# Optimization experiments

Measured on AMD Instinct MI355X. Metric: run time of the kernel, lower is better.

## Reference

```python
import jax, jax.numpy as jnp
import numpy as np

B, S, DIM, HEADS, MLP = 2, 2048, 1024, 16, 4096
DH = DIM // HEADS
LN_EPS = 1e-5


def layernorm(x, g, b):
    m = x.mean(-1, keepdims=True)
    v = ((x - m) ** 2).mean(-1, keepdims=True)
    return (x - m) / jnp.sqrt(v + LN_EPS) * g + b


def rope(x):
    # x: [B, H, S, dh]; interleaved-pair RoPE (rotary_embedding_torch convention)
    dh = x.shape[-1]
    s = x.shape[-2]
    inv_freq = 1.0 / (10000.0 ** (jnp.arange(0, dh, 2, dtype=jnp.float32) / dh))
    freqs = jnp.arange(s, dtype=jnp.float32)[:, None] * inv_freq[None, :]  # [S, dh/2]
    cos = jnp.repeat(jnp.cos(freqs), 2, axis=-1)  # [S, dh]
    sin = jnp.repeat(jnp.sin(freqs), 2, axis=-1)
    xp = x.reshape(x.shape[:-1] + (dh // 2, 2))
    x_rot = jnp.stack([-xp[..., 1], xp[..., 0]], axis=-1).reshape(x.shape)
    return x * cos + x_rot * sin


def setup_inputs() -> dict:
    key = jax.random.key(0)
    ks = jax.random.split(key, 10)
    w = 0.02
    return {
        "x": jax.random.normal(ks[0], (B, S, DIM), jnp.float32),
        "bias": jax.random.normal(ks[1], (B, S, S), jnp.float32) * 0.1,
        "ln1_g": jnp.ones((DIM,), jnp.float32),
        "ln1_b": jnp.zeros((DIM,), jnp.float32),
        "W_qkv": jax.random.normal(ks[2], (DIM, 3 * DIM), jnp.float32) * w,
        "W_o": jax.random.normal(ks[3], (DIM, DIM), jnp.float32) * w,
        "ln2_g": jnp.ones((DIM,), jnp.float32),
        "ln2_b": jnp.zeros((DIM,), jnp.float32),
        "W1": jax.random.normal(ks[4], (DIM, MLP), jnp.float32) * w,
        "b1": jnp.zeros((MLP,), jnp.float32),
        "W2": jax.random.normal(ks[5], (MLP, DIM), jnp.float32) * w,
        "b2": jnp.zeros((DIM,), jnp.float32),
        "pad_mask": jnp.zeros((B, S), jnp.int32),
    }


def reference(x, bias, ln1_g, ln1_b, W_qkv, W_o, ln2_g, ln2_b, W1, b1, W2, b2, pad_mask):
    b, s, d = x.shape
    h, dh = HEADS, DH
    res = x
    x1 = layernorm(x, ln1_g, ln1_b)
    qkv = (x1 @ W_qkv).reshape(b, s, h, 3 * dh)
    q, k, v = jnp.split(qkv, 3, axis=-1)            # each [B,S,H,dh]
    q = rope(q.transpose(0, 2, 1, 3))               # [B,H,S,dh]
    k = rope(k.transpose(0, 2, 1, 3))
    v = v.transpose(0, 2, 1, 3)
    scores = jnp.einsum("bhqd,bhkd->bhqk", q, k) * (dh ** -0.5)
    scores = scores + bias[:, None]                 # additive bias per batch
    key_mask = pad_mask.astype(bool)[:, None, None, :]
    scores = jnp.where(key_mask, -jnp.inf, scores)
    attn = jax.nn.softmax(scores, axis=-1)          # dropout = identity (eval)
    out = jnp.einsum("bhqk,bhkd->bhqd", attn, v)
    out = out.transpose(0, 2, 1, 3).reshape(b, s, d)
    x = res + out @ W_o
    res2 = x
    x2 = layernorm(x, ln2_g, ln2_b)
    mlp = jax.nn.gelu(x2 @ W1 + b1, approximate=False) @ W2 + b2
    return res2 + mlp
```

## Files before the change

kernel.cpp:

```cpp
#include <hip/hip_runtime.h>
#include <hip/hip_bf16.h>

#define B_   2
#define S_   2048
#define DIM_ 1024
#define H_   16
#define DH_  64
#define MLP_ 4096

typedef __bf16 bf16x8 __attribute__((ext_vector_type(8)));
typedef float  f32x4  __attribute__((ext_vector_type(4)));

__device__ __forceinline__ ushort f2bf(float f) {
    union { float f; unsigned u; } x; x.f = f;
    unsigned r = x.u + 0x7FFFu + ((x.u >> 16) & 1u);
    return (ushort)(r >> 16);
}
__device__ __forceinline__ float bf2f(ushort b) {
    union { unsigned u; float f; } x; x.u = ((unsigned)b) << 16;
    return x.f;
}

#define GLOAD_LDS16(gptr, lptr)                                                        \
    __builtin_amdgcn_global_load_lds(                                                  \
        (const __attribute__((address_space(1))) unsigned int*)(const void*)(gptr),    \
        (__attribute__((address_space(3))) unsigned int*)(void*)(lptr), 16, 0, 0)

#define MFMA_BF16(a, b, c) __builtin_amdgcn_mfma_f32_16x16x32_bf16((a), (b), (c), 0, 0, 0)

__global__ __launch_bounds__(256) void transpose_cvt(const float* __restrict__ in,
                                                     ushort* __restrict__ out,
                                                     int K, int N) {
    __shared__ float t[32][33];
    int n0 = blockIdx.x * 32, k0 = blockIdx.y * 32;
    int tx = threadIdx.x, ty = threadIdx.y;
#pragma unroll
    for (int r = 0; r < 32; r += 8)
        t[ty + r][tx] = in[(size_t)(k0 + ty + r) * N + n0 + tx];
    __syncthreads();
#pragma unroll
    for (int r = 0; r < 32; r += 8)
        out[(size_t)(n0 + ty + r) * K + k0 + tx] = f2bf(t[tx][ty + r]);
}

__global__ __launch_bounds__(256) void vt_prep(const ushort* __restrict__ qkv,
                                               ushort* __restrict__ VT) {
    __shared__ ushort t[32][34];
    int s0 = blockIdx.x * 32, d0 = blockIdx.y * 32, bh = blockIdx.z;
    int h = bh & 15, b = bh >> 4;
    const ushort* src = qkv + (size_t)b * S_ * (3 * DIM_) + h * 192 + 128;
    int tx = threadIdx.x, ty = threadIdx.y;
#pragma unroll
    for (int r = 0; r < 32; r += 8)
        t[ty + r][tx] = src[(size_t)(s0 + ty + r) * (3 * DIM_) + d0 + tx];
    __syncthreads();
    ushort* dst = VT + ((size_t)bh * DH_ + d0) * S_ + s0;
#pragma unroll
    for (int r = 0; r < 32; r += 8)
        dst[(size_t)(ty + r) * S_ + tx] = t[tx][ty + r];
}

__global__ __launch_bounds__(256) void ln_kernel(const float* __restrict__ in,
                                                 const float* __restrict__ g,
                                                 const float* __restrict__ beta,
                                                 ushort* __restrict__ out) {
    int row = blockIdx.x;
    float4 v = reinterpret_cast<const float4*>(in + (size_t)row * DIM_)[threadIdx.x];
    float s = v.x + v.y + v.z + v.w;
    float s2 = v.x * v.x + v.y * v.y + v.z * v.z + v.w * v.w;
#pragma unroll
    for (int m = 1; m < 64; m <<= 1) { s += __shfl_xor(s, m); s2 += __shfl_xor(s2, m); }
    __shared__ float red[8];
    int wid = threadIdx.x >> 6;
    if ((threadIdx.x & 63) == 0) { red[wid] = s; red[4 + wid] = s2; }
    __syncthreads();
    s  = red[0] + red[1] + red[2] + red[3];
    s2 = red[4] + red[5] + red[6] + red[7];
    float mean = s * (1.f / DIM_);
    float var  = s2 * (1.f / DIM_) - mean * mean;
    float inv  = rsqrtf(var + 1e-5f);
    float4 gg = reinterpret_cast<const float4*>(g)[threadIdx.x];
    float4 bb = reinterpret_cast<const float4*>(beta)[threadIdx.x];
    ushort4 o;
    o.x = f2bf((v.x - mean) * inv * gg.x + bb.x);
    o.y = f2bf((v.y - mean) * inv * gg.y + bb.y);
    o.z = f2bf((v.z - mean) * inv * gg.z + bb.z);
    o.w = f2bf((v.w - mean) * inv * gg.w + bb.w);
    reinterpret_cast<ushort4*>(out + (size_t)row * DIM_)[threadIdx.x] = o;
}

template <bool BIAS, bool GELU, bool RES, bool OBF16>
__global__ __launch_bounds__(256) void gemm_bt(const ushort* __restrict__ A,
                                               const ushort* __restrict__ Bt,
                                               void* __restrict__ Cout,
                                               const float* __restrict__ bias,
                                               const float* __restrict__ resid,
                                               int M, int N, int K) {
    __shared__ __align__(16) ushort As[2][128 * 32];
    __shared__ __align__(16) ushort Bs[2][128 * 32];
    int tid = threadIdx.x;
    int wid = tid >> 6, lane = tid & 63;
    int lr = lane & 15, lg = lane >> 4;

    int nbx = gridDim.x;
    int nwg = nbx * gridDim.y;
    int bid = blockIdx.y * nbx + blockIdx.x;
    int swz = (bid & 7) * (nwg >> 3) + (bid >> 3);
    int row0 = (swz / nbx) * 128, col0 = (swz % nbx) * 128;

    int wm = (wid >> 1) * 64, wn = (wid & 1) * 64;
    int srow = tid >> 2, scol = (tid & 3) * 8;

    f32x4 acc[4][4] = {};

    const ushort* ga0 = A + (size_t)(row0 + srow) * K + scol;
    const ushort* ga1 = A + (size_t)(row0 + 64 + srow) * K + scol;
    const ushort* gb0 = Bt + (size_t)(col0 + srow) * K + scol;
    const ushort* gb1 = Bt + (size_t)(col0 + 64 + srow) * K + scol;

    auto stage = [&](int buf, int kt) {
        ushort* a = As[buf] + wid * 512;
        ushort* b = Bs[buf] + wid * 512;
        GLOAD_LDS16(ga0 + kt, a);
        GLOAD_LDS16(ga1 + kt, a + 2048);
        GLOAD_LDS16(gb0 + kt, b);
        GLOAD_LDS16(gb1 + kt, b + 2048);
    };

    int nk = K >> 5;
    stage(0, 0);
    __syncthreads();

    for (int t = 0; t < nk; t++) {
        int cur = t & 1;
        if (t + 1 < nk) stage(cur ^ 1, (t + 1) << 5);
        bf16x8 af[4], bfr[4];
#pragma unroll
        for (int m = 0; m < 4; m++)
            af[m] = *reinterpret_cast<const bf16x8*>(As[cur] + (wm + m * 16 + lr) * 32 + lg * 8);
#pragma unroll
        for (int n = 0; n < 4; n++)
            bfr[n] = *reinterpret_cast<const bf16x8*>(Bs[cur] + (wn + n * 16 + lr) * 32 + lg * 8);
#pragma unroll
        for (int m = 0; m < 4; m++)
#pragma unroll
            for (int n = 0; n < 4; n++)
                acc[m][n] = MFMA_BF16(af[m], bfr[n], acc[m][n]);
        __syncthreads();
    }

#pragma unroll
    for (int m = 0; m < 4; m++) {
#pragma unroll
        for (int n = 0; n < 4; n++) {
            int col = col0 + wn + n * 16 + lr;
#pragma unroll
            for (int i = 0; i < 4; i++) {
                int row = row0 + wm + m * 16 + lg * 4 + i;
                float v = acc[m][n][i];
                if (BIAS) v += bias[col];
                if (GELU) v = 0.5f * v * (1.f + erff(v * 0.70710678118f));
                if (RES)  v += resid[(size_t)row * N + col];
                if (OBF16) ((ushort*)Cout)[(size_t)row * N + col] = f2bf(v);
                else       ((float*)Cout)[(size_t)row * N + col] = v;
            }
        }
    }
}

__global__ __launch_bounds__(256) void rope_table(float2* __restrict__ tab) {
    int i = blockIdx.x * 256 + threadIdx.x;
    int s = i >> 5, p = i & 31;
    float invf = __expf(-((float)(2 * p) / 64.f) * logf(10000.f));
    float a = (float)s * invf;
    tab[i] = make_float2(cosf(a), sinf(a));
}

__global__ __launch_bounds__(256) void rope_apply(const ushort* __restrict__ qkv,
                                                  const float2* __restrict__ tab,
                                                  ushort* __restrict__ Qo,
                                                  ushort* __restrict__ Ko) {
    int i = blockIdx.x * 256 + threadIdx.x;
    int p = i & 31;
    int s = (i >> 5) & (S_ - 1);
    int h = (i >> 16) & (H_ - 1);
    int b = i >> 20;
    float2 cs = tab[(s << 5) + p];
    size_t src = ((size_t)(b * S_ + s)) * (3 * DIM_) + h * 192 + 2 * p;
    size_t dst = (((size_t)(b * H_ + h) * S_) + s) * DH_ + 2 * p;
    float q0 = bf2f(qkv[src]), q1 = bf2f(qkv[src + 1]);
    Qo[dst]     = f2bf(q0 * cs.x - q1 * cs.y);
    Qo[dst + 1] = f2bf(q1 * cs.x + q0 * cs.y);
    float k0 = bf2f(qkv[src + 64]), k1 = bf2f(qkv[src + 65]);
    Ko[dst]     = f2bf(k0 * cs.x - k1 * cs.y);
    Ko[dst + 1] = f2bf(k1 * cs.x + k0 * cs.y);
}

__global__ __launch_bounds__(256) void attn_kernel(const ushort* __restrict__ Q,
                                                   const ushort* __restrict__ Kr,
                                                   const ushort* __restrict__ VT,
                                                   const float* __restrict__ bias,
                                                   const int* __restrict__ pad,
                                                   ushort* __restrict__ Out) {
    int bx = blockIdx.x;
    int qt = bx & 31, h = (bx >> 5) & 15, b = bx >> 9;
    __shared__ __align__(16) ushort Ks[64 * 72];
    __shared__ __align__(16) ushort Vs[64 * 72];
    __shared__ __align__(16) ushort Ps[64 * 72];
    int tid = threadIdx.x, wid = tid >> 6, lane = tid & 63;
    int lr = lane & 15, lg = lane >> 4;
    int q0 = qt * 64;
    const ushort* Qb = Q + ((size_t)(b * H_ + h) * S_) * DH_;
    const ushort* Kb = Kr + ((size_t)(b * H_ + h) * S_) * DH_;
    const ushort* Vb = VT + ((size_t)(b * H_ + h) * DH_) * S_;
    const float*  bb = bias + (size_t)b * S_ * S_;
    const int*    pb = pad + b * S_;

    bf16x8 qf[2];
#pragma unroll
    for (int ks = 0; ks < 2; ks++)
        qf[ks] = *reinterpret_cast<const bf16x8*>(
            Qb + (size_t)(q0 + wid * 16 + lr) * DH_ + ks * 32 + lg * 8);

    float mrow[4], lrow[4];
#pragma unroll
    for (int i = 0; i < 4; i++) { mrow[i] = -3e38f; lrow[i] = 0.f; }
    f32x4 o[4] = {};

    int sr = tid >> 3, sc = (tid & 7) * 8;
    const float scale = 0.125f;

    for (int kv0 = 0; kv0 < S_; kv0 += 64) {
        __syncthreads();
#pragma unroll
        for (int cc = 0; cc < 2; cc++) {
            int r = cc * 32 + sr;
            *reinterpret_cast<bf16x8*>(Ks + r * 72 + sc) =
                *reinterpret_cast<const bf16x8*>(Kb + (size_t)(kv0 + r) * DH_ + sc);
            *reinterpret_cast<bf16x8*>(Vs + r * 72 + sc) =
                *reinterpret_cast<const bf16x8*>(Vb + (size_t)r * S_ + kv0 + sc);
        }
        __syncthreads();

        f32x4 sa[4] = {};
#pragma unroll
        for (int n = 0; n < 4; n++) {
            bf16x8 k0 = *reinterpret_cast<const bf16x8*>(Ks + (n * 16 + lr) * 72 + lg * 8);
            bf16x8 k1 = *reinterpret_cast<const bf16x8*>(Ks + (n * 16 + lr) * 72 + 32 + lg * 8);
            sa[n] = MFMA_BF16(qf[0], k0, sa[n]);
            sa[n] = MFMA_BF16(qf[1], k1, sa[n]);
        }

        int pm[4];
#pragma unroll
        for (int n = 0; n < 4; n++) pm[n] = pb[kv0 + n * 16 + lr];

#pragma unroll
        for (int i = 0; i < 4; i++) {
            const float* brow = bb + (size_t)(q0 + wid * 16 + lg * 4 + i) * S_ + kv0;
            float sv[4];
            float rmax = -3e38f;
#pragma unroll
            for (int n = 0; n < 4; n++) {
                float s = sa[n][i] * scale + brow[n * 16 + lr];
                if (pm[n]) s = -1e30f;
                sv[n] = s;
                rmax = fmaxf(rmax, s);
            }
#pragma unroll
            for (int msk = 1; msk < 16; msk <<= 1) rmax = fmaxf(rmax, __shfl_xor(rmax, msk));
            float mnew = fmaxf(mrow[i], rmax);
            float resc = __expf(mrow[i] - mnew);
            mrow[i] = mnew;
            float ls = 0.f;
            int prow = (i << 2) | lg;
#pragma unroll
            for (int n = 0; n < 4; n++) {
                float p = __expf(sv[n] - mnew);
                ls += p;
                Ps[(wid * 16 + prow) * 72 + n * 16 + lr] = f2bf(p);
            }
            lrow[i] = lrow[i] * resc + ls;
#pragma unroll
            for (int fn = 0; fn < 4; fn++) o[fn][i] *= resc;
        }

        int plr = ((lr & 3) << 2) | (lr >> 2);
        bf16x8 pf0 = *reinterpret_cast<const bf16x8*>(Ps + (wid * 16 + plr) * 72 + lg * 8);
        bf16x8 pf1 = *reinterpret_cast<const bf16x8*>(Ps + (wid * 16 + plr) * 72 + 32 + lg * 8);

#pragma unroll
        for (int fn = 0; fn < 4; fn++) {
            bf16x8 v0 = *reinterpret_cast<const bf16x8*>(Vs + (fn * 16 + lr) * 72 + lg * 8);
            bf16x8 v1 = *reinterpret_cast<const bf16x8*>(Vs + (fn * 16 + lr) * 72 + 32 + lg * 8);
            o[fn] = MFMA_BF16(pf0, v0, o[fn]);
            o[fn] = MFMA_BF16(pf1, v1, o[fn]);
        }
    }

#pragma unroll
    for (int i = 0; i < 4; i++)
#pragma unroll
        for (int msk = 1; msk < 16; msk <<= 1) lrow[i] += __shfl_xor(lrow[i], msk);

#pragma unroll
    for (int fn = 0; fn < 4; fn++)
#pragma unroll
        for (int i = 0; i < 4; i++) {
            int qrow = q0 + wid * 16 + lg * 4 + i;
            Out[(size_t)(b * S_ + qrow) * DIM_ + h * DH_ + fn * 16 + lr] =
                f2bf(o[fn][i] / lrow[i]);
        }
}

extern "C" void kernel_launch(void* const* d_in, const int* in_sizes, int n_in,
                              void* d_out, int out_size, void* d_ws, size_t ws_size,
                              hipStream_t stream) {
    const float* x    = (const float*)d_in[0];
    const float* bias = (const float*)d_in[1];
    const float* ln1g = (const float*)d_in[2];
    const float* ln1b = (const float*)d_in[3];
    const float* Wqkv = (const float*)d_in[4];
    const float* Wo   = (const float*)d_in[5];
    const float* ln2g = (const float*)d_in[6];
    const float* ln2b = (const float*)d_in[7];
    const float* W1   = (const float*)d_in[8];
    const float* b1   = (const float*)d_in[9];
    const float* W2   = (const float*)d_in[10];
    const float* b2   = (const float*)d_in[11];
    const int*   pad  = (const int*)d_in[12];
    float* out = (float*)d_out;

    char* ws = (char*)d_ws;
    size_t off = 0;
    auto alloc = [&](size_t bytes) {
        char* p = ws + off;
        off += (bytes + 255) & ~(size_t)255;
        return (void*)p;
    };
    ushort* x1    = (ushort*)alloc((size_t)4096 * 1024 * 2);
    ushort* Wqkvt = (ushort*)alloc((size_t)3072 * 1024 * 2);
    ushort* qkv   = (ushort*)alloc((size_t)4096 * 3072 * 2);
    float2* tab   = (float2*)alloc((size_t)S_ * 32 * 8);
    ushort* Qr    = (ushort*)alloc((size_t)B_ * H_ * S_ * DH_ * 2);
    ushort* Kr2   = (ushort*)alloc((size_t)B_ * H_ * S_ * DH_ * 2);
    ushort* attnO = (ushort*)alloc((size_t)4096 * 1024 * 2);
    ushort* Wot   = (ushort*)alloc((size_t)1024 * 1024 * 2);
    float*  xmid  = (float*)alloc((size_t)4096 * 1024 * 4);
    ushort* x2    = (ushort*)alloc((size_t)4096 * 1024 * 2);
    ushort* W1t   = (ushort*)alloc((size_t)4096 * 1024 * 2);
    ushort* h1    = (ushort*)alloc((size_t)4096 * 4096 * 2);
    ushort* W2t   = (ushort*)alloc((size_t)1024 * 4096 * 2);
    ushort* VT    = h1;

    dim3 tb(32, 8);
    transpose_cvt<<<dim3(3072 / 32, 1024 / 32), tb, 0, stream>>>(Wqkv, Wqkvt, 1024, 3072);
    transpose_cvt<<<dim3(1024 / 32, 1024 / 32), tb, 0, stream>>>(Wo, Wot, 1024, 1024);
    transpose_cvt<<<dim3(4096 / 32, 1024 / 32), tb, 0, stream>>>(W1, W1t, 1024, 4096);
    transpose_cvt<<<dim3(1024 / 32, 4096 / 32), tb, 0, stream>>>(W2, W2t, 4096, 1024);

    ln_kernel<<<4096, 256, 0, stream>>>(x, ln1g, ln1b, x1);

    gemm_bt<false, false, false, true><<<dim3(3072 / 128, 4096 / 128), 256, 0, stream>>>(
        x1, Wqkvt, qkv, nullptr, nullptr, 4096, 3072, 1024);

    rope_table<<<(S_ * 32) / 256, 256, 0, stream>>>(tab);
    rope_apply<<<(B_ * H_ * S_ * 32) / 256, 256, 0, stream>>>(qkv, tab, Qr, Kr2);
    vt_prep<<<dim3(S_ / 32, DH_ / 32, B_ * H_), tb, 0, stream>>>(qkv, VT);

    attn_kernel<<<B_ * H_ * (S_ / 64), 256, 0, stream>>>(Qr, Kr2, VT, bias, pad, attnO);

    gemm_bt<false, false, true, false><<<dim3(1024 / 128, 4096 / 128), 256, 0, stream>>>(
        attnO, Wot, xmid, nullptr, x, 4096, 1024, 1024);

    ln_kernel<<<4096, 256, 0, stream>>>(xmid, ln2g, ln2b, x2);

    gemm_bt<true, true, false, true><<<dim3(4096 / 128, 4096 / 128), 256, 0, stream>>>(
        x2, W1t, h1, b1, nullptr, 4096, 4096, 1024);

    gemm_bt<true, false, true, false><<<dim3(1024 / 128, 4096 / 128), 256, 0, stream>>>(
        h1, W2t, out, b2, xmid, 4096, 1024, 4096);
}
```

Baseline: 356.7 us.

## Process two heads per attention block and share bias tile via LDS

The attention kernel now runs 512 threads per block covering two heads for the same query tile and batch. The additive bias tile (64x64 floats), which both heads need, is staged once per KV step into LDS with direct global-to-LDS loads, and each head reads it from there instead of from global memory. This halves global bias traffic, which is large (B*S*S floats read once per head). In exchange LDS use per block grows and the block is larger, which may lower occupancy.

New measurement: 378.6 us. 6.1% more time.

```diff
diff --git a/kernel.cpp b/kernel.cpp
--- a/kernel.cpp
+++ b/kernel.cpp
@@ -196,20 +196,24 @@
     Ko[dst + 1] = f2bf(k1 * cs.x + k0 * cs.y);
 }
 
-__global__ __launch_bounds__(256) void attn_kernel(const ushort* __restrict__ Q,
+__global__ __launch_bounds__(512) void attn_kernel(const ushort* __restrict__ Q,
                                                    const ushort* __restrict__ Kr,
                                                    const ushort* __restrict__ VT,
                                                    const float* __restrict__ bias,
                                                    const int* __restrict__ pad,
                                                    ushort* __restrict__ Out) {
     int bx = blockIdx.x;
-    int qt = bx & 31, h = (bx >> 5) & 15, b = bx >> 9;
-    __shared__ __align__(16) ushort Ks[64 * 72];
-    __shared__ __align__(16) ushort Vs[64 * 72];
-    __shared__ __align__(16) ushort Ps[64 * 72];
+    int qt = bx & 31, hp = (bx >> 5) & 7, b = bx >> 8;
+    __shared__ __align__(16) float  BsL[64 * 64];
+    __shared__ __align__(16) ushort Ks[2][64 * 72];
+    __shared__ __align__(16) ushort Vs[2][64 * 72];
+    __shared__ __align__(16) ushort Ps[2][64 * 72];
     int tid = threadIdx.x, wid = tid >> 6, lane = tid & 63;
+    int hh = tid >> 8;
+    int wid2 = wid & 3;
     int lr = lane & 15, lg = lane >> 4;
     int q0 = qt * 64;
+    int h = hp * 2 + hh;
     const ushort* Qb = Q + ((size_t)(b * H_ + h) * S_) * DH_;
     const ushort* Kb = Kr + ((size_t)(b * H_ + h) * S_) * DH_;
     const ushort* Vb = VT + ((size_t)(b * H_ + h) * DH_) * S_;
@@ -220,14 +224,15 @@
 #pragma unroll
     for (int ks = 0; ks < 2; ks++)
         qf[ks] = *reinterpret_cast<const bf16x8*>(
-            Qb + (size_t)(q0 + wid * 16 + lr) * DH_ + ks * 32 + lg * 8);
+            Qb + (size_t)(q0 + wid2 * 16 + lr) * DH_ + ks * 32 + lg * 8);
 
     float mrow[4], lrow[4];
 #pragma unroll
     for (int i = 0; i < 4; i++) { mrow[i] = -3e38f; lrow[i] = 0.f; }
     f32x4 o[4] = {};
 
-    int sr = tid >> 3, sc = (tid & 7) * 8;
+    int t2 = tid & 255;
+    int sr = t2 >> 3, sc = (t2 & 7) * 8;
     const float scale = 0.125f;
 
     for (int kv0 = 0; kv0 < S_; kv0 += 64) {
@@ -235,18 +240,24 @@
 #pragma unroll
         for (int cc = 0; cc < 2; cc++) {
             int r = cc * 32 + sr;
-            *reinterpret_cast<bf16x8*>(Ks + r * 72 + sc) =
+            *reinterpret_cast<bf16x8*>(Ks[hh] + r * 72 + sc) =
                 *reinterpret_cast<const bf16x8*>(Kb + (size_t)(kv0 + r) * DH_ + sc);
-            *reinterpret_cast<bf16x8*>(Vs + r * 72 + sc) =
+            *reinterpret_cast<bf16x8*>(Vs[hh] + r * 72 + sc) =
                 *reinterpret_cast<const bf16x8*>(Vb + (size_t)r * S_ + kv0 + sc);
         }
+#pragma unroll
+        for (int j2 = 0; j2 < 2; j2++) {
+            int j = wid * 2 + j2;
+            GLOAD_LDS16(bb + (size_t)(q0 + 4 * j + (lane >> 4)) * S_ + kv0 + (lane & 15) * 4,
+                        BsL + j * 256);
+        }
         __syncthreads();
 
         f32x4 sa[4] = {};
 #pragma unroll
         for (int n = 0; n < 4; n++) {
-            bf16x8 k0 = *reinterpret_cast<const bf16x8*>(Ks + (n * 16 + lr) * 72 + lg * 8);
-            bf16x8 k1 = *reinterpret_cast<const bf16x8*>(Ks + (n * 16 + lr) * 72 + 32 + lg * 8);
+            bf16x8 k0 = *reinterpret_cast<const bf16x8*>(Ks[hh] + (n * 16 + lr) * 72 + lg * 8);
+            bf16x8 k1 = *reinterpret_cast<const bf16x8*>(Ks[hh] + (n * 16 + lr) * 72 + 32 + lg * 8);
             sa[n] = MFMA_BF16(qf[0], k0, sa[n]);
             sa[n] = MFMA_BF16(qf[1], k1, sa[n]);
         }
@@ -257,7 +268,7 @@
 
 #pragma unroll
         for (int i = 0; i < 4; i++) {
-            const float* brow = bb + (size_t)(q0 + wid * 16 + lg * 4 + i) * S_ + kv0;
+            const float* brow = BsL + (wid2 * 16 + lg * 4 + i) * 64;
             float sv[4];
             float rmax = -3e38f;
 #pragma unroll
@@ -278,7 +289,7 @@
             for (int n = 0; n < 4; n++) {
                 float p = __expf(sv[n] - mnew);
                 ls += p;
-                Ps[(wid * 16 + prow) * 72 + n * 16 + lr] = f2bf(p);
+                Ps[hh][(wid2 * 16 + prow) * 72 + n * 16 + lr] = f2bf(p);
             }
             lrow[i] = lrow[i] * resc + ls;
 #pragma unroll
@@ -286,13 +297,13 @@
         }
 
         int plr = ((lr & 3) << 2) | (lr >> 2);
-        bf16x8 pf0 = *reinterpret_cast<const bf16x8*>(Ps + (wid * 16 + plr) * 72 + lg * 8);
-        bf16x8 pf1 = *reinterpret_cast<const bf16x8*>(Ps + (wid * 16 + plr) * 72 + 32 + lg * 8);
+        bf16x8 pf0 = *reinterpret_cast<const bf16x8*>(Ps[hh] + (wid2 * 16 + plr) * 72 + lg * 8);
+        bf16x8 pf1 = *reinterpret_cast<const bf16x8*>(Ps[hh] + (wid2 * 16 + plr) * 72 + 32 + lg * 8);
 
 #pragma unroll
         for (int fn = 0; fn < 4; fn++) {
-            bf16x8 v0 = *reinterpret_cast<const bf16x8*>(Vs + (fn * 16 + lr) * 72 + lg * 8);
-            bf16x8 v1 = *reinterpret_cast<const bf16x8*>(Vs + (fn * 16 + lr) * 72 + 32 + lg * 8);
+            bf16x8 v0 = *reinterpret_cast<const bf16x8*>(Vs[hh] + (fn * 16 + lr) * 72 + lg * 8);
+            bf16x8 v1 = *reinterpret_cast<const bf16x8*>(Vs[hh] + (fn * 16 + lr) * 72 + 32 + lg * 8);
             o[fn] = MFMA_BF16(pf0, v0, o[fn]);
             o[fn] = MFMA_BF16(pf1, v1, o[fn]);
         }
@@ -307,7 +318,7 @@
     for (int fn = 0; fn < 4; fn++)
 #pragma unroll
         for (int i = 0; i < 4; i++) {
-            int qrow = q0 + wid * 16 + lg * 4 + i;
+            int qrow = q0 + wid2 * 16 + lg * 4 + i;
             Out[(size_t)(b * S_ + qrow) * DIM_ + h * DH_ + fn * 16 + lr] =
                 f2bf(o[fn][i] / lrow[i]);
         }
@@ -368,7 +379,7 @@
     rope_apply<<<(B_ * H_ * S_ * 32) / 256, 256, 0, stream>>>(qkv, tab, Qr, Kr2);
     vt_prep<<<dim3(S_ / 32, DH_ / 32, B_ * H_), tb, 0, stream>>>(qkv, VT);
 
-    attn_kernel<<<B_ * H_ * (S_ / 64), 256, 0, stream>>>(Qr, Kr2, VT, bias, pad, attnO);
+    attn_kernel<<<B_ * (H_ / 2) * (S_ / 64), 512, 0, stream>>>(Qr, Kr2, VT, bias, pad, attnO);
 
     gemm_bt<false, false, true, false><<<dim3(1024 / 128, 4096 / 128), 256, 0, stream>>>(
         attnO, Wot, xmid, nullptr, x, 4096, 1024, 1024);
```
